# Kernel tuning notes

Hardware: AMD Instinct MI355X
Metric: run time of the kernel (lower is better)

## Reference

```python
import jax, jax.numpy as jnp
import numpy as np

EPS = float(np.finfo(np.float64).eps)  # np.finfo(float).eps as in torch combine


def setup_inputs() -> dict:
    key = jax.random.key(0)
    ks = jax.random.split(key, 4)
    B, E, D_in, D_h, D_out = 4096, 8, 768, 2048, 768
    return {
        "x": jax.random.normal(ks[0], (B, D_in), dtype=jnp.float32),
        "w_gate": jax.random.normal(ks[1], (D_in, E), dtype=jnp.float32) * 0.02,
        "W1": jax.random.normal(ks[2], (E, D_in, D_h), dtype=jnp.float32) * (1.0 / np.sqrt(D_in)),
        "b1": jnp.zeros((E, D_h), dtype=jnp.float32),
        "W2": jax.random.normal(ks[3], (E, D_h, D_out), dtype=jnp.float32) * (1.0 / np.sqrt(D_h)),
        "b2": jnp.zeros((E, D_out), dtype=jnp.float32),
        "k": 2,
    }


def _cv_squared(v):
    # torch .var() is unbiased (ddof=1)
    return jnp.var(v, ddof=1) / (jnp.mean(v) ** 2 + 1e-10)


def _top_k_gates(logits, k):
    B, E = logits.shape
    top_vals, top_idx = jax.lax.top_k(logits, k)        # [B, k]
    top_gates = jax.nn.softmax(top_vals, axis=1)        # softmax over the k kept logits
    gates = jnp.zeros((B, E), logits.dtype).at[jnp.arange(B)[:, None], top_idx].set(top_gates)
    return gates


def reference(x, w_gate, W1, b1, W2, b2, k):
    # --- gating (eval path: noiseless clean logits, softmax gating) ---
    logits = x @ w_gate                                  # [B, E]
    gates = _top_k_gates(logits, k)                      # [B, E], sparse (k nonzeros/row)
    # --- per-expert MLP: Linear -> gelu -> Linear -> log_softmax ---
    # Dense grouped compute over experts; gate==0 terms contribute nothing in combine.
    h = jax.nn.gelu(jnp.einsum('bi,eih->beh', x, W1) + b1[None])      # [B, E, Dh]
    lo = jax.nn.log_softmax(jnp.einsum('beh,eho->beo', h, W2) + b2[None], axis=-1)  # [B, E, Do]
    # --- combine: exp, weight by gates, scatter-add, eps-clamp, log ---
    combined = jnp.einsum('be,beo->bo', gates, jnp.exp(lo))           # [B, Do]
    y = jnp.log(jnp.where(combined == 0, EPS, combined))
    # --- load-balancing aux loss (eval: load = count of nonzero gates) ---
    importance = gates.sum(0)
    load = (gates > 0).sum(0).astype(jnp.float32)
    loss = 0.01 * (_cv_squared(importance) + _cv_squared(load))
    return y, loss
```

## Files before the change

kernel.cpp:

```cpp
#include <hip/hip_runtime.h>
#include <hip/hip_bf16.h>
#include <math.h>

typedef __hip_bfloat16 bf16;
typedef short v8s __attribute__((ext_vector_type(8)));
typedef float v4f __attribute__((ext_vector_type(4)));

#define B_TOK 4096
#define E_EXP 8
#define D_IN  768
#define D_H   2048
#define D_OUT 768

__device__ __forceinline__ void gl_lds16(const bf16* g, bf16* l) {
  __builtin_amdgcn_global_load_lds(
      (const __attribute__((address_space(1))) unsigned int*)g,
      (__attribute__((address_space(3))) unsigned int*)l, 16, 0, 0);
}

__global__ void gate_cvt_kernel(const float* __restrict__ x, const float* __restrict__ wg,
                                bf16* __restrict__ xb,
                                float* __restrict__ gates, int* __restrict__ tidx) {
  int gt = blockIdx.x * 256 + threadIdx.x;
  int tok = gt >> 6, l = gt & 63;
  const float* xr = x + (size_t)tok * D_IN;
  bf16* xbr = xb + (size_t)tok * D_IN;
  float acc[8] = {0.f,0.f,0.f,0.f,0.f,0.f,0.f,0.f};
  #pragma unroll
  for (int i = 0; i < 3; ++i) {
    int k0 = i * 256 + l * 4;
    float4 v = *(const float4*)(xr + k0);
    union { bf16 h[4]; uint2 u; } pk;
    pk.h[0] = __float2bfloat16(v.x); pk.h[1] = __float2bfloat16(v.y);
    pk.h[2] = __float2bfloat16(v.z); pk.h[3] = __float2bfloat16(v.w);
    *(uint2*)(xbr + k0) = pk.u;
    float xv[4] = {v.x, v.y, v.z, v.w};
    #pragma unroll
    for (int j = 0; j < 4; ++j) {
      const float* wr = wg + (size_t)(k0 + j) * 8;
      float4 w0 = *(const float4*)wr;
      float4 w1 = *(const float4*)(wr + 4);
      acc[0] += xv[j] * w0.x; acc[1] += xv[j] * w0.y;
      acc[2] += xv[j] * w0.z; acc[3] += xv[j] * w0.w;
      acc[4] += xv[j] * w1.x; acc[5] += xv[j] * w1.y;
      acc[6] += xv[j] * w1.z; acc[7] += xv[j] * w1.w;
    }
  }
  #pragma unroll
  for (int d = 1; d < 64; d <<= 1)
    #pragma unroll
    for (int e = 0; e < 8; ++e) acc[e] += __shfl_xor(acc[e], d);
  if (l == 0) {
    int i1 = 0; float v1 = acc[0];
    #pragma unroll
    for (int e = 1; e < 8; ++e) if (acc[e] > v1) { v1 = acc[e]; i1 = e; }
    int i2 = -1; float v2 = -1e30f;
    #pragma unroll
    for (int e = 0; e < 8; ++e) if (e != i1 && acc[e] > v2) { v2 = acc[e]; i2 = e; }
    float ex = __expf(v2 - v1);
    float g1 = 1.f / (1.f + ex), g2 = ex / (1.f + ex);
    gates[2 * tok] = g1; gates[2 * tok + 1] = g2;
    tidx[2 * tok] = i1;  tidx[2 * tok + 1] = i2;
  }
}

__global__ void finalize_kernel(const int* __restrict__ tidx, const float* __restrict__ gates,
                                int* __restrict__ cnt_off, int* __restrict__ row_ids,
                                int* __restrict__ pos, float* __restrict__ loss_out) {
  __shared__ int   hcnt[256][9];
  __shared__ float himp[256][9];
  __shared__ int   tot[8], off[8];
  __shared__ float itot[8];
  int t = threadIdx.x;
  #pragma unroll
  for (int e = 0; e < 8; ++e) { hcnt[t][e] = 0; himp[t][e] = 0.f; }
  __syncthreads();
  for (int i = 0; i < 32; ++i) {
    int idx = t * 32 + i;
    int e = tidx[idx];
    hcnt[t][e] += 1;
    himp[t][e] += gates[idx];
  }
  __syncthreads();
  if (t < 8) {
    int run = 0; float s = 0.f;
    for (int j = 0; j < 256; ++j) {
      int c = hcnt[j][t];
      hcnt[j][t] = run;
      run += c;
      s += himp[j][t];
    }
    tot[t] = run; itot[t] = s;
  }
  __syncthreads();
  if (t == 0) {
    int o = 0;
    float mi = 0.f, ml = 0.f;
    for (int e = 0; e < 8; ++e) {
      off[e] = o; o += tot[e];
      cnt_off[e] = tot[e]; cnt_off[8 + e] = off[e];
      mi += itot[e]; ml += (float)tot[e];
    }
    mi *= 0.125f; ml *= 0.125f;
    float vi = 0.f, vl = 0.f;
    for (int e = 0; e < 8; ++e) {
      float d = itot[e] - mi;        vi += d * d;
      float d2 = (float)tot[e] - ml; vl += d2 * d2;
    }
    vi /= 7.f; vl /= 7.f;
    *loss_out = 0.01f * (vi / (mi * mi + 1e-10f) + vl / (ml * ml + 1e-10f));
  }
  __syncthreads();
  for (int i = 0; i < 32; ++i) {
    int idx = t * 32 + i;
    int e = tidx[idx];
    int slot = off[e] + hcnt[t][e];
    hcnt[t][e] += 1;
    row_ids[slot] = idx >> 1;
    pos[idx] = slot;
  }
}

__global__ void transpose_cvt(const float* __restrict__ W, bf16* __restrict__ Wt,
                              int K, int N) {
  __shared__ bf16 tile[64][72];
  int e = blockIdx.z;
  int k0 = blockIdx.y * 64, n0 = blockIdx.x * 64;
  const float* Wp = W + (size_t)e * K * N;
  bf16* Wtp = Wt + (size_t)e * N * K;
  int t = threadIdx.x;
  int cr = t >> 4;
  int cc = (t & 15) * 4;
  #pragma unroll
  for (int p = 0; p < 4; ++p) {
    int kr = cr + p * 16;
    float4 v = *(const float4*)(Wp + (size_t)(k0 + kr) * N + n0 + cc);
    tile[cc + 0][kr] = __float2bfloat16(v.x);
    tile[cc + 1][kr] = __float2bfloat16(v.y);
    tile[cc + 2][kr] = __float2bfloat16(v.z);
    tile[cc + 3][kr] = __float2bfloat16(v.w);
  }
  __syncthreads();
  #pragma unroll
  for (int p = 0; p < 2; ++p) {
    int o = p * 256 + t;
    int n = o >> 3, k8 = (o & 7) * 8;
    v8s val = *(const v8s*)&tile[n][k8];
    *(v8s*)(Wtp + (size_t)(n0 + n) * K + k0 + k8) = val;
  }
}

template<int KDIM, int BM, bool GATHER, bool GELU>
__global__ __launch_bounds__(256)
void gemm_mlp(const bf16* __restrict__ Ab, const bf16* __restrict__ Wt,
              const float* __restrict__ bias, bf16* __restrict__ Outb,
              const int* __restrict__ row_ids, const int* __restrict__ cnt_off,
              const int N) {
  constexpr int BK = 64;
  constexpr int BN = 128;
  constexpr int ITA = BM / 32;
  constexpr int FM  = BM / 32;
  __shared__ __align__(16) bf16 lsA[BM * BK];
  __shared__ __align__(16) bf16 lsB[BN * BK];
  const int e = blockIdx.z;
  const int cnt = cnt_off[e];
  const int rowb = blockIdx.y;
  if (rowb * BM >= cnt) return;
  const int off = cnt_off[8 + e];
  const int colb = blockIdx.x;
  const int t = (int)threadIdx.x, w = t >> 6, l = t & 63;
  const int cs = (l & 7) ^ (l >> 3);
  const bf16* gA[ITA];
  const bf16* gB[4];
  #pragma unroll
  for (int it = 0; it < ITA; ++it) {
    int rt = (it * 4 + w) * 8 + (l >> 3);
    int r = rowb * BM + rt;
    int rc = r < cnt ? r : cnt - 1;
    long arow = GATHER ? (long)row_ids[off + rc] : (long)(off + rc);
    gA[it] = Ab + arow * (long)KDIM + cs * 8;
  }
  #pragma unroll
  for (int it = 0; it < 4; ++it) {
    int rt = (it * 4 + w) * 8 + (l >> 3);
    gB[it] = Wt + ((size_t)e * N + (size_t)colb * BN + rt) * KDIM + cs * 8;
  }
  v4f acc[FM][4] = {};
  const int wm = w >> 1, wn = w & 1;
  for (int ks = 0; ks < KDIM / BK; ++ks) {
    const int k0 = ks * BK;
    #pragma unroll
    for (int it = 0; it < ITA; ++it) gl_lds16(gA[it] + k0, lsA + (it * 4 + w) * 512);
    #pragma unroll
    for (int it = 0; it < 4; ++it)   gl_lds16(gB[it] + k0, lsB + (it * 4 + w) * 512);
    __syncthreads();
    #pragma unroll
    for (int kk = 0; kk < 2; ++kk) {
      v8s af[FM], bfr[4];
      #pragma unroll
      for (int fm = 0; fm < FM; ++fm) {
        int row = wm * (BM / 2) + fm * 16 + (l & 15);
        int cg = kk * 4 + (l >> 4);
        af[fm] = *(const v8s*)(lsA + row * BK + ((cg ^ (row & 7)) << 3));
      }
      #pragma unroll
      for (int fn = 0; fn < 4; ++fn) {
        int row = wn * 64 + fn * 16 + (l & 15);
        int cg = kk * 4 + (l >> 4);
        bfr[fn] = *(const v8s*)(lsB + row * BK + ((cg ^ (row & 7)) << 3));
      }
      #pragma unroll
      for (int fm = 0; fm < FM; ++fm)
        #pragma unroll
        for (int fn = 0; fn < 4; ++fn)
          acc[fm][fn] = __builtin_amdgcn_mfma_f32_16x16x32_bf16(af[fm], bfr[fn], acc[fm][fn], 0, 0, 0);
    }
    __syncthreads();
  }
  const float* bp = bias + (size_t)e * N + (size_t)colb * BN;
  #pragma unroll
  for (int fm = 0; fm < FM; ++fm) {
    int lr0 = wm * (BM / 2) + fm * 16 + (l >> 4) * 4;
    #pragma unroll
    for (int fn = 0; fn < 4; ++fn) {
      int lcol = wn * 64 + fn * 16 + (l & 15);
      float bv = bp[lcol];
      #pragma unroll
      for (int q = 0; q < 4; ++q) {
        int lr = lr0 + q;
        int r = rowb * BM + lr;
        if (r < cnt) {
          float v = acc[fm][fn][q] + bv;
          if (GELU) {
            float u = 0.7978845608028654f * (v + 0.044715f * v * v * v);
            float th = 1.f - 2.f / (__expf(2.f * u) + 1.f);
            v = 0.5f * v * (1.f + th);
          }
          Outb[(size_t)(off + r) * N + (size_t)colb * BN + lcol] = __float2bfloat16(v);
        }
      }
    }
  }
}

__global__ void combine_kernel(const bf16* __restrict__ z, const float* __restrict__ gates,
                               const int* __restrict__ pos, float* __restrict__ y) {
  int gt = blockIdx.x * 256 + threadIdx.x;
  int tok = gt >> 6, l = gt & 63;
  if (tok >= B_TOK) return;
  const bf16* z1 = z + (size_t)pos[2 * tok] * D_OUT;
  const bf16* z2 = z + (size_t)pos[2 * tok + 1] * D_OUT;
  float g1 = gates[2 * tok], g2 = gates[2 * tok + 1];
  float a[12], b[12];
  float m1 = -1e30f, m2 = -1e30f;
  #pragma unroll
  for (int i = 0; i < 12; ++i) {
    a[i] = __bfloat162float(z1[l + 64 * i]);
    b[i] = __bfloat162float(z2[l + 64 * i]);
    m1 = fmaxf(m1, a[i]); m2 = fmaxf(m2, b[i]);
  }
  #pragma unroll
  for (int d = 1; d < 64; d <<= 1) {
    m1 = fmaxf(m1, __shfl_xor(m1, d));
    m2 = fmaxf(m2, __shfl_xor(m2, d));
  }
  float s1 = 0.f, s2 = 0.f;
  #pragma unroll
  for (int i = 0; i < 12; ++i) { s1 += __expf(a[i] - m1); s2 += __expf(b[i] - m2); }
  #pragma unroll
  for (int d = 1; d < 64; d <<= 1) { s1 += __shfl_xor(s1, d); s2 += __shfl_xor(s2, d); }
  float c1 = g1 / s1, c2 = g2 / s2;
  #pragma unroll
  for (int i = 0; i < 12; ++i) {
    float cmb = c1 * __expf(a[i] - m1) + c2 * __expf(b[i] - m2);
    y[(size_t)tok * D_OUT + l + 64 * i] = logf(cmb == 0.f ? 2.2204460492503131e-16f : cmb);
  }
}

extern "C" void kernel_launch(void* const* d_in, const int* in_sizes, int n_in,
                              void* d_out, int out_size, void* d_ws, size_t ws_size,
                              hipStream_t stream) {
  const float* x  = (const float*)d_in[0];
  const float* wg = (const float*)d_in[1];
  const float* W1 = (const float*)d_in[2];
  const float* b1 = (const float*)d_in[3];
  const float* W2 = (const float*)d_in[4];
  const float* b2 = (const float*)d_in[5];
  float* out = (float*)d_out;

  char* ws = (char*)d_ws;
  int*   cnt_off = (int*)(ws + 0);
  float* gates   = (float*)(ws + 256);
  int*   tidx    = (int*)(ws + 256 + 32768);
  int*   pos     = (int*)(ws + 256 + 65536);
  int*   row_ids = (int*)(ws + 256 + 98304);
  const size_t base = 262144;
  bf16* x_bf = (bf16*)(ws + base);
  bf16* W1t  = (bf16*)(ws + base + 6291456);
  bf16* W2t  = (bf16*)(ws + base + 31457280);
  bf16* h_bf = (bf16*)(ws + base + 56623104);
  bf16* z_bf = (bf16*)(ws + base);

  transpose_cvt<<<dim3(D_H / 64,  D_IN / 64, E_EXP), 256, 0, stream>>>(W1, W1t, D_IN, D_H);
  transpose_cvt<<<dim3(D_OUT / 64, D_H / 64, E_EXP), 256, 0, stream>>>(W2, W2t, D_H, D_OUT);
  gate_cvt_kernel<<<dim3(1024), 256, 0, stream>>>(x, wg, x_bf, gates, tidx);
  finalize_kernel<<<dim3(1), 256, 0, stream>>>(tidx, gates, cnt_off, row_ids, pos,
                                               out + (size_t)B_TOK * D_OUT);
  gemm_mlp<D_IN, 128, true,  true ><<<dim3(D_H / 128,  64, E_EXP), 256, 0, stream>>>(
      x_bf, W1t, b1, h_bf, row_ids, cnt_off, D_H);
  gemm_mlp<D_H,  64,  false, false><<<dim3(D_OUT / 128, 128, E_EXP), 256, 0, stream>>>(
      h_bf, W2t, b2, z_bf, row_ids, cnt_off, D_OUT);
  combine_kernel<<<dim3(1024), 256, 0, stream>>>(z_bf, gates, pos, out);
}
```

Baseline: 194.8 us.

## Double-buffer LDS in grouped GEMM and compact tile grid via tile map

```diff
diff --git a/kernel.cpp b/kernel.cpp
--- a/kernel.cpp
+++ b/kernel.cpp
@@ -11,6 +11,7 @@
 #define D_IN  768
 #define D_H   2048
 #define D_OUT 768
+#define MAXT  72
 
 __device__ __forceinline__ void gl_lds16(const bf16* g, bf16* l) {
   __builtin_amdgcn_global_load_lds(
@@ -66,7 +67,8 @@
 
 __global__ void finalize_kernel(const int* __restrict__ tidx, const float* __restrict__ gates,
                                 int* __restrict__ cnt_off, int* __restrict__ row_ids,
-                                int* __restrict__ pos, float* __restrict__ loss_out) {
+                                int* __restrict__ pos, int* __restrict__ tmap,
+                                float* __restrict__ loss_out) {
   __shared__ int   hcnt[256][9];
   __shared__ float himp[256][9];
   __shared__ int   tot[8], off[8];
@@ -109,6 +111,12 @@
     }
     vi /= 7.f; vl /= 7.f;
     *loss_out = 0.01f * (vi / (mi * mi + 1e-10f) + vl / (ml * ml + 1e-10f));
+    int nt = 0;
+    for (int e = 0; e < 8; ++e)
+      for (int tt = 0; tt < (tot[e] + 127) >> 7; ++tt) {
+        tmap[nt] = e; tmap[MAXT + nt] = tt; ++nt;
+      }
+    for (; nt < MAXT; ++nt) tmap[nt] = -1;
   }
   __syncthreads();
   for (int i = 0; i < 32; ++i) {
@@ -150,30 +158,30 @@
   }
 }
 
-template<int KDIM, int BM, bool GATHER, bool GELU>
+template<int KDIM, bool GATHER, bool GELU>
 __global__ __launch_bounds__(256)
 void gemm_mlp(const bf16* __restrict__ Ab, const bf16* __restrict__ Wt,
               const float* __restrict__ bias, bf16* __restrict__ Outb,
               const int* __restrict__ row_ids, const int* __restrict__ cnt_off,
-              const int N) {
-  constexpr int BK = 64;
-  constexpr int BN = 128;
-  constexpr int ITA = BM / 32;
-  constexpr int FM  = BM / 32;
-  __shared__ __align__(16) bf16 lsA[BM * BK];
-  __shared__ __align__(16) bf16 lsB[BN * BK];
-  const int e = blockIdx.z;
+              const int* __restrict__ tmap, const int N) {
+  constexpr int BK = 64, BM = 128, BN = 128;
+  constexpr int NK = KDIM / BK;
+  static_assert(NK % 2 == 0, "NK even");
+  __shared__ __align__(16) bf16 lsA0[BM * BK], lsB0[BN * BK];
+  __shared__ __align__(16) bf16 lsA1[BM * BK], lsB1[BN * BK];
+  const int ti = blockIdx.y;
+  const int e = tmap[ti];
+  if (e < 0) return;
+  const int rowb = tmap[MAXT + ti];
   const int cnt = cnt_off[e];
-  const int rowb = blockIdx.y;
-  if (rowb * BM >= cnt) return;
   const int off = cnt_off[8 + e];
   const int colb = blockIdx.x;
   const int t = (int)threadIdx.x, w = t >> 6, l = t & 63;
   const int cs = (l & 7) ^ (l >> 3);
-  const bf16* gA[ITA];
+  const bf16* gA[4];
   const bf16* gB[4];
   #pragma unroll
-  for (int it = 0; it < ITA; ++it) {
+  for (int it = 0; it < 4; ++it) {
     int rt = (it * 4 + w) * 8 + (l >> 3);
     int r = rowb * BM + rt;
     int rc = r < cnt ? r : cnt - 1;
@@ -185,42 +193,58 @@
     int rt = (it * 4 + w) * 8 + (l >> 3);
     gB[it] = Wt + ((size_t)e * N + (size_t)colb * BN + rt) * KDIM + cs * 8;
   }
-  v4f acc[FM][4] = {};
+  v4f acc[4][4] = {};
   const int wm = w >> 1, wn = w & 1;
-  for (int ks = 0; ks < KDIM / BK; ++ks) {
-    const int k0 = ks * BK;
-    #pragma unroll
-    for (int it = 0; it < ITA; ++it) gl_lds16(gA[it] + k0, lsA + (it * 4 + w) * 512);
-    #pragma unroll
-    for (int it = 0; it < 4; ++it)   gl_lds16(gB[it] + k0, lsB + (it * 4 + w) * 512);
+
+#define STAGE(lA, lB, k0) do {                                             \
+    _Pragma("unroll")                                                      \
+    for (int it = 0; it < 4; ++it) gl_lds16(gA[it] + (k0), (lA) + (it * 4 + w) * 512); \
+    _Pragma("unroll")                                                      \
+    for (int it = 0; it < 4; ++it) gl_lds16(gB[it] + (k0), (lB) + (it * 4 + w) * 512); \
+  } while (0)
+
+#define COMPUTE(lA, lB) do {                                               \
+    _Pragma("unroll")                                                      \
+    for (int kk = 0; kk < 2; ++kk) {                                       \
+      v8s af[4], bfr[4];                                                   \
+      _Pragma("unroll")                                                    \
+      for (int fm = 0; fm < 4; ++fm) {                                     \
+        int row = wm * 64 + fm * 16 + (l & 15);                            \
+        int cg = kk * 4 + (l >> 4);                                        \
+        af[fm] = *(const v8s*)((lA) + row * BK + ((cg ^ (row & 7)) << 3)); \
+      }                                                                    \
+      _Pragma("unroll")                                                    \
+      for (int fn = 0; fn < 4; ++fn) {                                     \
+        int row = wn * 64 + fn * 16 + (l & 15);                            \
+        int cg = kk * 4 + (l >> 4);                                        \
+        bfr[fn] = *(const v8s*)((lB) + row * BK + ((cg ^ (row & 7)) << 3));\
+      }                                                                    \
+      _Pragma("unroll")                                                    \
+      for (int fm = 0; fm < 4; ++fm)                                       \
+        _Pragma("unroll")                                                  \
+        for (int fn = 0; fn < 4; ++fn)                                     \
+          acc[fm][fn] = __builtin_amdgcn_mfma_f32_16x16x32_bf16(af[fm], bfr[fn], acc[fm][fn], 0, 0, 0); \
+    }                                                                      \
+  } while (0)
+
+  STAGE(lsA0, lsB0, 0);
+  __syncthreads();
+  #pragma unroll 1
+  for (int ks = 0; ks < NK; ks += 2) {
+    if (ks + 1 < NK) STAGE(lsA1, lsB1, (ks + 1) * BK);
+    COMPUTE(lsA0, lsB0);
     __syncthreads();
-    #pragma unroll
-    for (int kk = 0; kk < 2; ++kk) {
-      v8s af[FM], bfr[4];
-      #pragma unroll
-      for (int fm = 0; fm < FM; ++fm) {
-        int row = wm * (BM / 2) + fm * 16 + (l & 15);
-        int cg = kk * 4 + (l >> 4);
-        af[fm] = *(const v8s*)(lsA + row * BK + ((cg ^ (row & 7)) << 3));
-      }
-      #pragma unroll
-      for (int fn = 0; fn < 4; ++fn) {
-        int row = wn * 64 + fn * 16 + (l & 15);
-        int cg = kk * 4 + (l >> 4);
-        bfr[fn] = *(const v8s*)(lsB + row * BK + ((cg ^ (row & 7)) << 3));
-      }
-      #pragma unroll
-      for (int fm = 0; fm < FM; ++fm)
-        #pragma unroll
-        for (int fn = 0; fn < 4; ++fn)
-          acc[fm][fn] = __builtin_amdgcn_mfma_f32_16x16x32_bf16(af[fm], bfr[fn], acc[fm][fn], 0, 0, 0);
-    }
+    if (ks + 2 < NK) STAGE(lsA0, lsB0, (ks + 2) * BK);
+    COMPUTE(lsA1, lsB1);
     __syncthreads();
   }
+#undef STAGE
+#undef COMPUTE
+
   const float* bp = bias + (size_t)e * N + (size_t)colb * BN;
   #pragma unroll
-  for (int fm = 0; fm < FM; ++fm) {
-    int lr0 = wm * (BM / 2) + fm * 16 + (l >> 4) * 4;
+  for (int fm = 0; fm < 4; ++fm) {
+    int lr0 = wm * 64 + fm * 16 + (l >> 4) * 4;
     #pragma unroll
     for (int fn = 0; fn < 4; ++fn) {
       int lcol = wn * 64 + fn * 16 + (l & 15);
@@ -294,6 +318,7 @@
   int*   tidx    = (int*)(ws + 256 + 32768);
   int*   pos     = (int*)(ws + 256 + 65536);
   int*   row_ids = (int*)(ws + 256 + 98304);
+  int*   tmap    = (int*)(ws + 256 + 131072);
   const size_t base = 262144;
   bf16* x_bf = (bf16*)(ws + base);
   bf16* W1t  = (bf16*)(ws + base + 6291456);
@@ -304,11 +329,11 @@
   transpose_cvt<<<dim3(D_H / 64,  D_IN / 64, E_EXP), 256, 0, stream>>>(W1, W1t, D_IN, D_H);
   transpose_cvt<<<dim3(D_OUT / 64, D_H / 64, E_EXP), 256, 0, stream>>>(W2, W2t, D_H, D_OUT);
   gate_cvt_kernel<<<dim3(1024), 256, 0, stream>>>(x, wg, x_bf, gates, tidx);
-  finalize_kernel<<<dim3(1), 256, 0, stream>>>(tidx, gates, cnt_off, row_ids, pos,
+  finalize_kernel<<<dim3(1), 256, 0, stream>>>(tidx, gates, cnt_off, row_ids, pos, tmap,
                                                out + (size_t)B_TOK * D_OUT);
-  gemm_mlp<D_IN, 128, true,  true ><<<dim3(D_H / 128,  64, E_EXP), 256, 0, stream>>>(
-      x_bf, W1t, b1, h_bf, row_ids, cnt_off, D_H);
-  gemm_mlp<D_H,  64,  false, false><<<dim3(D_OUT / 128, 128, E_EXP), 256, 0, stream>>>(
-      h_bf, W2t, b2, z_bf, row_ids, cnt_off, D_OUT);
+  gemm_mlp<D_IN, true,  true ><<<dim3(D_H / 128,  MAXT), 256, 0, stream>>>(
+      x_bf, W1t, b1, h_bf, row_ids, cnt_off, tmap, D_H);
+  gemm_mlp<D_H,  false, false><<<dim3(D_OUT / 128, MAXT), 256, 0, stream>>>(
+      h_bf, W2t, b2, z_bf, row_ids, cnt_off, tmap, D_OUT);
   combine_kernel<<<dim3(1024), 256, 0, stream>>>(z_bf, gates, pos, out);
 }
```

After: 181.0 us. -7.0%, faster.
